# Optimization experiments

Hardware: AMD Instinct MI355X
Metric: run time of the kernel (lower is better)

The kernel has to match this reference:

```python
import jax, jax.numpy as jnp
import numpy as np

N = 100000       # num nodes
E = 3200000      # num edges (avg degree 32)
F_IN = 128       # num_node_features
HID = 16         # hidden dim hard-coded in Net
C = 10           # num_classes


def setup_inputs() -> dict:
    key = jax.random.key(0)
    k1, k2, k3, k4 = jax.random.split(key, 4)
    x = jax.random.normal(k1, (N, F_IN), dtype=jnp.float32)
    edge_index = jax.random.randint(k2, (2, E), 0, N, dtype=jnp.int32)
    W1 = jax.random.normal(k3, (F_IN, HID), dtype=jnp.float32) * 0.05
    b1 = jnp.zeros((HID,), dtype=jnp.float32)
    W2 = jax.random.normal(k4, (HID, C), dtype=jnp.float32) * 0.05
    b2 = jnp.zeros((C,), dtype=jnp.float32)
    return {"x": x, "edge_index": edge_index, "W1": W1, "b1": b1, "W2": W2, "b2": b2}


def reference(x, edge_index, W1, b1, W2, b2):
    # GCNConv: out = D^{-1/2} (A + I) D^{-1/2} X W + b   (add self-loops)
    loops = jnp.arange(N, dtype=edge_index.dtype)
    row = jnp.concatenate([edge_index[0], loops])  # source nodes
    col = jnp.concatenate([edge_index[1], loops])  # target nodes

    # symmetric normalization (degrees include self-loops, so deg >= 1)
    deg = jax.ops.segment_sum(jnp.ones_like(col, dtype=jnp.float32), col, num_segments=N)
    dis = jax.lax.rsqrt(deg)
    norm = dis[row] * dis[col]  # [E+N]

    def gcn_conv(h, W, b):
        h = h @ W                               # [N, d_out] small GEMM first
        msg = h[row] * norm[:, None]            # gather + scale, [E+N, d_out]
        out = jax.ops.segment_sum(msg, col, num_segments=N)  # scatter-add
        return out + b

    h = jax.nn.relu(gcn_conv(x, W1, b1))
    # F.dropout(training=False) is identity in eval mode
    logits = gcn_conv(h, W2, b2)
    return jax.nn.log_softmax(logits, axis=1)
```

## Files before the change

kernel.cpp:

```cpp
#include <hip/hip_runtime.h>
#include <math.h>

#define N_NODES 100000
#define N_EDGES 3200000
#define F_IN 128
#define HID 16
#define C_OUT 10
#define WIN 256
#define NDIG 391
#define PNB2 500
#define EPB 6400
#define SCN (NDIG * PNB2)
#define SB1 764
#define MAXE2 20
#define CSRLDS 10240

typedef unsigned short u16;
typedef unsigned int u32;

__device__ __forceinline__ float bf2f(u16 u) {
    return __uint_as_float(((u32)u) << 16);
}
__device__ __forceinline__ u16 f2bf(float f) {
    u32 x = __float_as_uint(f);
    u32 r = (x + 0x7fffu + ((x >> 16) & 1u)) >> 16;
    return (u16)r;
}
__device__ __forceinline__ void acc8(float* a, uint4 w) {
    a[0] += bf2f((u16)(w.x & 0xffff)); a[1] += bf2f((u16)(w.x >> 16));
    a[2] += bf2f((u16)(w.y & 0xffff)); a[3] += bf2f((u16)(w.y >> 16));
    a[4] += bf2f((u16)(w.z & 0xffff)); a[5] += bf2f((u16)(w.z >> 16));
    a[6] += bf2f((u16)(w.w & 0xffff)); a[7] += bf2f((u16)(w.w >> 16));
}

__global__ void k_pcnt(const int* __restrict__ col, int* __restrict__ blkhistA) {
    __shared__ int h[NDIG];
    for (int i = threadIdx.x; i < NDIG; i += 256) h[i] = 0;
    __syncthreads();
    const uint4* c4 = (const uint4*)(col + blockIdx.x * EPB);
    for (int i = threadIdx.x; i < EPB / 4; i += 256) {
        uint4 c = c4[i];
        atomicAdd(&h[c.x >> 8], 1);
        atomicAdd(&h[c.y >> 8], 1);
        atomicAdd(&h[c.z >> 8], 1);
        atomicAdd(&h[c.w >> 8], 1);
    }
    __syncthreads();
    for (int d = threadIdx.x; d < NDIG; d += 256)
        blkhistA[d * PNB2 + blockIdx.x] = h[d];
}

__global__ void k_s1(const int* __restrict__ blkhistA, int* __restrict__ psum) {
    __shared__ int sm[256];
    int i = blockIdx.x * 256 + threadIdx.x;
    sm[threadIdx.x] = (i < SCN) ? blkhistA[i] : 0;
    __syncthreads();
    for (int off = 128; off > 0; off >>= 1) {
        if (threadIdx.x < off) sm[threadIdx.x] += sm[threadIdx.x + off];
        __syncthreads();
    }
    if (threadIdx.x == 0) psum[blockIdx.x] = sm[0];
}

__global__ void k_s3(const int* __restrict__ blkhistA, const int* __restrict__ psum,
                     int* __restrict__ blkhistB) {
    __shared__ int ps[1024];
    __shared__ int sm[256];
    int t = threadIdx.x;
    for (int i = t; i < 1024; i += 256) ps[i] = (i < SB1) ? psum[i] : 0;
    __syncthreads();
    for (int off = 1; off < 1024; off <<= 1) {
        int v[4];
#pragma unroll
        for (int j = 0; j < 4; j++) {
            int idx = t + j * 256;
            v[j] = ps[idx] + ((idx >= off) ? ps[idx - off] : 0);
        }
        __syncthreads();
#pragma unroll
        for (int j = 0; j < 4; j++) ps[t + j * 256] = v[j];
        __syncthreads();
    }
    int bpre = (blockIdx.x > 0) ? ps[blockIdx.x - 1] : 0;

    int i = blockIdx.x * 256 + t;
    int v = (i < SCN) ? blkhistA[i] : 0;
    sm[t] = v;
    __syncthreads();
    for (int off = 1; off < 256; off <<= 1) {
        int a = sm[t];
        int b = (t >= off) ? sm[t - off] : 0;
        __syncthreads();
        sm[t] = a + b;
        __syncthreads();
    }
    if (i < SCN) blkhistB[i] = bpre + sm[t] - v;
}

__global__ void __launch_bounds__(512) k_pwrite(
        const int* __restrict__ row, const int* __restrict__ col,
        const int* __restrict__ blkhistA, const int* __restrict__ blkhistB,
        u32* __restrict__ staging) {
    __shared__ u32 sorted[EPB];
    __shared__ u16 dwin[EPB];
    __shared__ int gbase[NDIG];
    __shared__ int lbase[NDIG];
    __shared__ int lcur[NDIG];
    __shared__ int scan[512];

    int t = threadIdx.x;
    int b = blockIdx.x;
    int hv = 0;
    if (t < NDIG) {
        hv = blkhistA[t * PNB2 + b];
        gbase[t] = blkhistB[t * PNB2 + b];
        lcur[t] = 0;
    }
    scan[t] = hv;
    __syncthreads();
    for (int off = 1; off < 512; off <<= 1) {
        int v = scan[t];
        int u = (t >= off) ? scan[t - off] : 0;
        __syncthreads();
        scan[t] = v + u;
        __syncthreads();
    }
    if (t < NDIG) lbase[t] = scan[t] - hv;
    __syncthreads();

    const uint4* c4 = (const uint4*)(col + b * EPB);
    const uint4* r4 = (const uint4*)(row + b * EPB);
    for (int i = t; i < EPB / 4; i += 512) {
        uint4 c = c4[i];
        uint4 r = r4[i];
        int d, rank, pos;
        d = (int)(c.x >> 8); rank = atomicAdd(&lcur[d], 1); pos = lbase[d] + rank;
        sorted[pos] = ((c.x & 255u) << 17) | r.x; dwin[pos] = (u16)d;
        d = (int)(c.y >> 8); rank = atomicAdd(&lcur[d], 1); pos = lbase[d] + rank;
        sorted[pos] = ((c.y & 255u) << 17) | r.y; dwin[pos] = (u16)d;
        d = (int)(c.z >> 8); rank = atomicAdd(&lcur[d], 1); pos = lbase[d] + rank;
        sorted[pos] = ((c.z & 255u) << 17) | r.z; dwin[pos] = (u16)d;
        d = (int)(c.w >> 8); rank = atomicAdd(&lcur[d], 1); pos = lbase[d] + rank;
        sorted[pos] = ((c.w & 255u) << 17) | r.w; dwin[pos] = (u16)d;
    }
    __syncthreads();

    for (int i = t; i < EPB; i += 512) {
        int d = dwin[i];
        staging[gbase[d] + (i - lbase[d])] = sorted[i];
    }
}

__global__ void __launch_bounds__(256) k_gemm1d(
        const float* __restrict__ x, const float* __restrict__ W1,
        const u32* __restrict__ staging, const int* __restrict__ blkhistB,
        float* __restrict__ dis, u16* __restrict__ h1s) {
    __shared__ float Ws[F_IN * HID];
    __shared__ int cnt[WIN];
    int w = blockIdx.x;
    int t = threadIdx.x;
    for (int i = t; i < F_IN * HID; i += 256) Ws[i] = W1[i];
    cnt[t] = 0;
    __syncthreads();
    int start = blkhistB[w * PNB2];
    int end = (w == NDIG - 1) ? N_EDGES : blkhistB[(w + 1) * PNB2];
    int head = (4 - (start & 3)) & 3;
    if (head > end - start) head = end - start;
    if (t < head) atomicAdd(&cnt[staging[start + t] >> 17], 1);
    int abody = start + head;
    int nb = (end - abody) >> 2;
    const uint4* s4 = (const uint4*)(staging + abody);
    for (int i = t; i < nb; i += 256) {
        uint4 e = s4[i];
        atomicAdd(&cnt[e.x >> 17], 1);
        atomicAdd(&cnt[e.y >> 17], 1);
        atomicAdd(&cnt[e.z >> 17], 1);
        atomicAdd(&cnt[e.w >> 17], 1);
    }
    int tstart = abody + (nb << 2);
    if (t < end - tstart) atomicAdd(&cnt[staging[tstart + t] >> 17], 1);
    __syncthreads();

    int node = w * WIN + t;
    if (node >= N_NODES) return;
    float d = rsqrtf(1.0f + (float)cnt[t]);
    dis[node] = d;

    float acc[HID];
#pragma unroll
    for (int j = 0; j < HID; j++) acc[j] = 0.f;

    const float4* xr = (const float4*)(x + (size_t)node * F_IN);
#pragma unroll 2
    for (int k4 = 0; k4 < F_IN / 4; k4++) {
        float4 v = xr[k4];
        float xv[4] = {v.x, v.y, v.z, v.w};
#pragma unroll
        for (int kk = 0; kk < 4; kk++) {
            const float4* wr = (const float4*)(Ws + (k4 * 4 + kk) * HID);
            float4 w0 = wr[0], w1 = wr[1], w2 = wr[2], w3 = wr[3];
            float xs = xv[kk];
            acc[0]  += xs * w0.x; acc[1]  += xs * w0.y; acc[2]  += xs * w0.z; acc[3]  += xs * w0.w;
            acc[4]  += xs * w1.x; acc[5]  += xs * w1.y; acc[6]  += xs * w1.z; acc[7]  += xs * w1.w;
            acc[8]  += xs * w2.x; acc[9]  += xs * w2.y; acc[10] += xs * w2.z; acc[11] += xs * w2.w;
            acc[12] += xs * w3.x; acc[13] += xs * w3.y; acc[14] += xs * w3.z; acc[15] += xs * w3.w;
        }
    }

    u32 p[8];
#pragma unroll
    for (int i = 0; i < 8; i++)
        p[i] = (u32)f2bf(acc[2 * i] * d) | ((u32)f2bf(acc[2 * i + 1] * d) << 16);
    u32* dst = (u32*)(h1s + (size_t)node * HID);
#pragma unroll
    for (int i = 0; i < 8; i++) dst[i] = p[i];
}

__global__ void __launch_bounds__(512) k_gl1f(
        u32* staging, const int* __restrict__ blkhistB,
        const u16* __restrict__ h1s, const float* __restrict__ b1,
        const float* __restrict__ W2,
        int* __restrict__ offs, uint4* __restrict__ h2a, u32* __restrict__ h2b) {
    __shared__ u32 sorted[CSRLDS];
    __shared__ int cnt[WIN];
    __shared__ int sbase[WIN];
    __shared__ int cur[WIN];
    __shared__ float Ws[HID * C_OUT];
    __shared__ float b1s[HID];
    int w = blockIdx.x;
    int t = threadIdx.x;
    if (t < HID * C_OUT) Ws[t] = W2[t];
    if (t < HID) b1s[t] = b1[t];
    if (t < WIN) cnt[t] = 0;
    __syncthreads();
    int start = blkhistB[w * PNB2];
    int end = (w == NDIG - 1) ? N_EDGES : blkhistB[(w + 1) * PNB2];
    int m = end - start;
    u32 buf[MAXE2];
    int n = 0;
#pragma unroll
    for (int k = 0; k < MAXE2; k++) {
        int i = k * 512 + t;
        if (i < m) {
            u32 e = staging[start + i];
            buf[k] = e;
            n = k + 1;
            atomicAdd(&cnt[e >> 17], 1);
        }
    }
    __syncthreads();
    if (t < WIN) sbase[t] = cnt[t];
    __syncthreads();
    for (int off = 1; off < WIN; off <<= 1) {
        int v = 0;
        if (t < WIN) {
            v = sbase[t];
            if (t >= off) v += sbase[t - off];
        }
        __syncthreads();
        if (t < WIN) sbase[t] = v;
        __syncthreads();
    }
    if (t < WIN) {
        int excl = sbase[t] - cnt[t];
        sbase[t] = excl;
        cur[t] = excl;
        int node = w * WIN + t;
        if (node < N_NODES) offs[node] = start + excl;
    }
    if (w == 0 && t == 0) offs[N_NODES] = N_EDGES;
    __syncthreads();
#pragma unroll
    for (int k = 0; k < MAXE2; k++) {
        if (k < n) {
            u32 e = buf[k];
            int pos = atomicAdd(&cur[(int)(e >> 17)], 1);
            sorted[pos] = e;
        }
    }
    __syncthreads();
    for (int i = t; i < m; i += 512)
        staging[start + i] = sorted[i];

    const uint4* hb = (const uint4*)h1s;
    int half = (t >> 2) & 1;
    int eq = t & 3;
#pragma unroll 1
    for (int rep = 0; rep < 4; rep++) {
        int nl = rep * 64 + (t >> 3);
        int node = w * WIN + nl;
        bool valid = node < N_NODES;
        float a[8] = {0.f, 0.f, 0.f, 0.f, 0.f, 0.f, 0.f, 0.f};
        int deg = valid ? cnt[nl] : 0;
        int s0 = sbase[nl];
        if (valid && eq == 0) acc8(a, hb[(size_t)node * 2 + half]);
        int lo = s0 + ((deg * eq) >> 2);
        int hi = s0 + ((deg * (eq + 1)) >> 2);
        int j = lo;
        for (; j + 4 <= hi; j += 4) {
            u32 e0 = sorted[j], e1 = sorted[j + 1], e2 = sorted[j + 2], e3 = sorted[j + 3];
            uint4 w0 = hb[(size_t)(e0 & 0x1FFFFu) * 2 + half];
            uint4 w1 = hb[(size_t)(e1 & 0x1FFFFu) * 2 + half];
            uint4 w2 = hb[(size_t)(e2 & 0x1FFFFu) * 2 + half];
            uint4 w3 = hb[(size_t)(e3 & 0x1FFFFu) * 2 + half];
            acc8(a, w0); acc8(a, w1); acc8(a, w2); acc8(a, w3);
        }
        for (; j < hi; j++)
            acc8(a, hb[(size_t)(sorted[j] & 0x1FFFFu) * 2 + half]);

#pragma unroll
        for (int k = 0; k < 8; k++) {
            a[k] += __shfl_xor(a[k], 1);
            a[k] += __shfl_xor(a[k], 2);
        }

        float dc = rsqrtf(1.0f + (float)deg);
        float own[8], oth[8];
#pragma unroll
        for (int k = 0; k < 8; k++) own[k] = a[k] * dc;
#pragma unroll
        for (int k = 0; k < 8; k++) oth[k] = __shfl_xor(own[k], 4);
        float h[16];
#pragma unroll
        for (int k = 0; k < 8; k++) {
            h[k]     = half ? oth[k] : own[k];
            h[8 + k] = half ? own[k] : oth[k];
        }
#pragma unroll
        for (int jj = 0; jj < 16; jj++) h[jj] = fmaxf(h[jj] + b1s[jj], 0.f);

        int nf = half ? 2 : 8;
        float outv[8];
#pragma unroll
        for (int k = 0; k < 8; k++) {
            float s = 0.f;
            if (k < nf) {
                int kk = half * 8 + k;
#pragma unroll
                for (int jj = 0; jj < 16; jj++) s += h[jj] * Ws[jj * C_OUT + kk];
            }
            outv[k] = s * dc;
        }
        if (valid && eq == 0) {
            if (half == 0) {
                uint4 ov;
                ov.x = (u32)f2bf(outv[0]) | ((u32)f2bf(outv[1]) << 16);
                ov.y = (u32)f2bf(outv[2]) | ((u32)f2bf(outv[3]) << 16);
                ov.z = (u32)f2bf(outv[4]) | ((u32)f2bf(outv[5]) << 16);
                ov.w = (u32)f2bf(outv[6]) | ((u32)f2bf(outv[7]) << 16);
                h2a[node] = ov;
            } else {
                h2b[node] = (u32)f2bf(outv[0]) | ((u32)f2bf(outv[1]) << 16);
            }
        }
    }
}

__global__ void k_gather2(const int* __restrict__ offs, const u32* __restrict__ csr,
                          const float* __restrict__ dis, const uint4* __restrict__ h2a,
                          const u32* __restrict__ h2b,
                          const float* __restrict__ b2, float* __restrict__ out) {
    __shared__ float b2s[C_OUT];
    if (threadIdx.x < C_OUT) b2s[threadIdx.x] = b2[threadIdx.x];
    __syncthreads();

    int t = blockIdx.x * 256 + threadIdx.x;
    if (t >= N_NODES * 8) return;
    int node = t >> 3;
    int q = t & 7;
    int half = q >> 2;
    int eq = q & 3;
    float a[8] = {0.f, 0.f, 0.f, 0.f, 0.f, 0.f, 0.f, 0.f};
    if (eq == 0) {
        if (half == 0) {
            acc8(a, h2a[node]);
        } else {
            u32 sc = h2b[node];
            a[0] += bf2f((u16)(sc & 0xffff));
            a[1] += bf2f((u16)(sc >> 16));
        }
    }
    int o = offs[node + half];
    int oo = __shfl_xor(o, 4);
    int s0 = half ? oo : o;
    int s1 = half ? o : oo;
    int len = s1 - s0;
    int lo = s0 + ((len * eq) >> 2);
    int hi = s0 + ((len * (eq + 1)) >> 2);
    int j = lo;
    for (; j < hi && (j & 3); j++) {
        u32 src = csr[j] & 0x1FFFFu;
        if (half == 0) {
            acc8(a, h2a[src]);
        } else {
            u32 v = h2b[src];
            a[0] += bf2f((u16)(v & 0xffff));
            a[1] += bf2f((u16)(v >> 16));
        }
    }
    for (; j + 4 <= hi; j += 4) {
        uint4 ss = *(const uint4*)(csr + j);
        u32 i0 = ss.x & 0x1FFFFu, i1 = ss.y & 0x1FFFFu;
        u32 i2 = ss.z & 0x1FFFFu, i3 = ss.w & 0x1FFFFu;
        if (half == 0) {
            uint4 w0 = h2a[i0];
            uint4 w1 = h2a[i1];
            uint4 w2 = h2a[i2];
            uint4 w3 = h2a[i3];
            acc8(a, w0); acc8(a, w1); acc8(a, w2); acc8(a, w3);
        } else {
            u32 v0 = h2b[i0], v1 = h2b[i1], v2 = h2b[i2], v3 = h2b[i3];
            a[0] += bf2f((u16)(v0 & 0xffff)); a[1] += bf2f((u16)(v0 >> 16));
            a[0] += bf2f((u16)(v1 & 0xffff)); a[1] += bf2f((u16)(v1 >> 16));
            a[0] += bf2f((u16)(v2 & 0xffff)); a[1] += bf2f((u16)(v2 >> 16));
            a[0] += bf2f((u16)(v3 & 0xffff)); a[1] += bf2f((u16)(v3 >> 16));
        }
    }
    for (; j < hi; j++) {
        u32 src = csr[j] & 0x1FFFFu;
        if (half == 0) {
            acc8(a, h2a[src]);
        } else {
            u32 v = h2b[src];
            a[0] += bf2f((u16)(v & 0xffff));
            a[1] += bf2f((u16)(v >> 16));
        }
    }

#pragma unroll
    for (int k = 0; k < 8; k++) {
        a[k] += __shfl_xor(a[k], 1);
        a[k] += __shfl_xor(a[k], 2);
    }

    float dc = dis[node];
    int nf = half ? 2 : 8;
    int fb = half * 8;
    float lg[8];
    float m = -1e30f;
#pragma unroll
    for (int k = 0; k < 8; k++) {
        if (k < nf) {
            lg[k] = a[k] * dc + b2s[fb + k];
            m = fmaxf(m, lg[k]);
        }
    }
    m = fmaxf(m, __shfl_xor(m, 4));
    float s = 0.f;
#pragma unroll
    for (int k = 0; k < 8; k++)
        if (k < nf) s += expf(lg[k] - m);
    s += __shfl_xor(s, 4);
    float ls = logf(s) + m;
    if (eq == 0) {
        float* dst = out + (size_t)node * C_OUT + half * 8;
        if (half == 0) {
#pragma unroll
            for (int i = 0; i < 4; i++)
                *(float2*)(dst + 2 * i) = make_float2(lg[2 * i] - ls, lg[2 * i + 1] - ls);
        } else {
            *(float2*)dst = make_float2(lg[0] - ls, lg[1] - ls);
        }
    }
}

extern "C" void kernel_launch(void* const* d_in, const int* in_sizes, int n_in,
                              void* d_out, int out_size, void* d_ws, size_t ws_size,
                              hipStream_t stream) {
    const float* x  = (const float*)d_in[0];
    const int*   ei = (const int*)d_in[1];
    const float* W1 = (const float*)d_in[2];
    const float* b1 = (const float*)d_in[3];
    const float* W2 = (const float*)d_in[4];
    const float* b2 = (const float*)d_in[5];
    float* out = (float*)d_out;

    const int* row = ei;
    const int* col = ei + N_EDGES;

    char* ws = (char*)d_ws;
    float* dis      = (float*)(ws);
    int*   offs     = (int*)(ws + 400000);
    int*   blkhistA = (int*)(ws + 800016);
    int*   blkhistB = (int*)(ws + 1582352);
    int*   psum     = (int*)(ws + 2364688);
    u32*   staging  = (u32*)(ws + 2367744);
    u16*   h1s      = (u16*)(ws + 15167744);
    uint4* h2a      = (uint4*)(ws + 18367744);
    u32*   h2b      = (u32*)(ws + 19967744);

    const int B = 256;
    int gN8 = (N_NODES * 8 + B - 1) / B;

    k_pcnt  <<<PNB2, B, 0, stream>>>(col, blkhistA);
    k_s1    <<<SB1, B, 0, stream>>>(blkhistA, psum);
    k_s3    <<<SB1, B, 0, stream>>>(blkhistA, psum, blkhistB);
    k_pwrite<<<PNB2, 512, 0, stream>>>(row, col, blkhistA, blkhistB, staging);
    k_gemm1d<<<NDIG, B, 0, stream>>>(x, W1, staging, blkhistB, dis, h1s);
    k_gl1f  <<<NDIG, 512, 0, stream>>>(staging, blkhistB, h1s, b1, W2, offs, h2a, h2b);
    k_gather2<<<gN8, B, 0, stream>>>(offs, staging, dis, h2a, h2b, b2, out);
}
```

Before: 213.8 us.

## Overlap layer-1 GEMM with histogram pass and compute degrees via global atomics

Merges the column histogram kernel with the X·W1 GEMM into one launch of heterogeneous blocks, so the dense GEMM runs alongside the edge histogram instead of after the partition write. Degrees are now counted with global atomics during the histogram pass rather than from the sorted staging buffer. The dis scaling and bf16 packing move into a second kernel that also holds the partial-sum reduction. In exchange it adds 3.2M global atomics, a memset, and an fp32 intermediate written and read back through memory.

```diff
diff --git a/kernel.cpp b/kernel.cpp
--- a/kernel.cpp
+++ b/kernel.cpp
@@ -33,33 +33,99 @@
     a[6] += bf2f((u16)(w.w & 0xffff)); a[7] += bf2f((u16)(w.w >> 16));
 }
 
-__global__ void k_pcnt(const int* __restrict__ col, int* __restrict__ blkhistA) {
-    __shared__ int h[NDIG];
-    for (int i = threadIdx.x; i < NDIG; i += 256) h[i] = 0;
-    __syncthreads();
-    const uint4* c4 = (const uint4*)(col + blockIdx.x * EPB);
-    for (int i = threadIdx.x; i < EPB / 4; i += 256) {
-        uint4 c = c4[i];
-        atomicAdd(&h[c.x >> 8], 1);
-        atomicAdd(&h[c.y >> 8], 1);
-        atomicAdd(&h[c.z >> 8], 1);
-        atomicAdd(&h[c.w >> 8], 1);
-    }
-    __syncthreads();
-    for (int d = threadIdx.x; d < NDIG; d += 256)
-        blkhistA[d * PNB2 + blockIdx.x] = h[d];
-}
-
-__global__ void k_s1(const int* __restrict__ blkhistA, int* __restrict__ psum) {
-    __shared__ int sm[256];
-    int i = blockIdx.x * 256 + threadIdx.x;
-    sm[threadIdx.x] = (i < SCN) ? blkhistA[i] : 0;
-    __syncthreads();
-    for (int off = 128; off > 0; off >>= 1) {
-        if (threadIdx.x < off) sm[threadIdx.x] += sm[threadIdx.x + off];
-        __syncthreads();
-    }
-    if (threadIdx.x == 0) psum[blockIdx.x] = sm[0];
+__global__ void __launch_bounds__(256) k_front(
+        const int* __restrict__ col, const float* __restrict__ x,
+        const float* __restrict__ W1,
+        int* __restrict__ blkhistA, u32* __restrict__ deg, float* __restrict__ h1u) {
+    __shared__ float WsF[F_IN * HID];
+    int t = threadIdx.x;
+    if (blockIdx.x < PNB2) {
+        int* h = (int*)WsF;
+        for (int i = t; i < NDIG; i += 256) h[i] = 0;
+        __syncthreads();
+        const uint4* c4 = (const uint4*)(col + blockIdx.x * EPB);
+        for (int i = t; i < EPB / 4; i += 256) {
+            uint4 c = c4[i];
+            atomicAdd(&h[c.x >> 8], 1);
+            atomicAdd(&h[c.y >> 8], 1);
+            atomicAdd(&h[c.z >> 8], 1);
+            atomicAdd(&h[c.w >> 8], 1);
+            atomicAdd(&deg[c.x], 1u);
+            atomicAdd(&deg[c.y], 1u);
+            atomicAdd(&deg[c.z], 1u);
+            atomicAdd(&deg[c.w], 1u);
+        }
+        __syncthreads();
+        for (int d = t; d < NDIG; d += 256)
+            blkhistA[d * PNB2 + blockIdx.x] = h[d];
+    } else {
+        for (int i = t; i < F_IN * HID; i += 256) WsF[i] = W1[i];
+        __syncthreads();
+        int node = (blockIdx.x - PNB2) * 256 + t;
+        if (node >= N_NODES) return;
+
+        float acc[HID];
+#pragma unroll
+        for (int j = 0; j < HID; j++) acc[j] = 0.f;
+        const float4* xr = (const float4*)(x + (size_t)node * F_IN);
+#pragma unroll 2
+        for (int k4 = 0; k4 < F_IN / 4; k4++) {
+            float4 v = xr[k4];
+            float xv[4] = {v.x, v.y, v.z, v.w};
+#pragma unroll
+            for (int kk = 0; kk < 4; kk++) {
+                const float4* wr = (const float4*)(WsF + (k4 * 4 + kk) * HID);
+                float4 w0 = wr[0], w1 = wr[1], w2 = wr[2], w3 = wr[3];
+                float xs = xv[kk];
+                acc[0]  += xs * w0.x; acc[1]  += xs * w0.y; acc[2]  += xs * w0.z; acc[3]  += xs * w0.w;
+                acc[4]  += xs * w1.x; acc[5]  += xs * w1.y; acc[6]  += xs * w1.z; acc[7]  += xs * w1.w;
+                acc[8]  += xs * w2.x; acc[9]  += xs * w2.y; acc[10] += xs * w2.z; acc[11] += xs * w2.w;
+                acc[12] += xs * w3.x; acc[13] += xs * w3.y; acc[14] += xs * w3.z; acc[15] += xs * w3.w;
+            }
+        }
+        float4* dst = (float4*)(h1u + (size_t)node * HID);
+#pragma unroll
+        for (int i = 0; i < 4; i++)
+            dst[i] = make_float4(acc[4 * i], acc[4 * i + 1], acc[4 * i + 2], acc[4 * i + 3]);
+    }
+}
+
+__global__ void __launch_bounds__(256) k_mid(
+        const int* __restrict__ blkhistA, int* __restrict__ psum,
+        const u32* __restrict__ deg, const float* __restrict__ h1u,
+        float* __restrict__ dis, u16* __restrict__ h1s) {
+    int t = threadIdx.x;
+    if (blockIdx.x < SB1) {
+        __shared__ int sm[256];
+        int i = blockIdx.x * 256 + t;
+        sm[t] = (i < SCN) ? blkhistA[i] : 0;
+        __syncthreads();
+        for (int off = 128; off > 0; off >>= 1) {
+            if (t < off) sm[t] += sm[t + off];
+            __syncthreads();
+        }
+        if (t == 0) psum[blockIdx.x] = sm[0];
+    } else {
+        int node = (blockIdx.x - SB1) * 256 + t;
+        if (node >= N_NODES) return;
+        float d = rsqrtf(1.0f + (float)deg[node]);
+        dis[node] = d;
+        const float4* src = (const float4*)(h1u + (size_t)node * HID);
+        float4 v0 = src[0], v1 = src[1], v2 = src[2], v3 = src[3];
+        float v[16] = {v0.x, v0.y, v0.z, v0.w, v1.x, v1.y, v1.z, v1.w,
+                       v2.x, v2.y, v2.z, v2.w, v3.x, v3.y, v3.z, v3.w};
+        uint4 p0, p1;
+        p0.x = (u32)f2bf(v[0] * d)  | ((u32)f2bf(v[1] * d) << 16);
+        p0.y = (u32)f2bf(v[2] * d)  | ((u32)f2bf(v[3] * d) << 16);
+        p0.z = (u32)f2bf(v[4] * d)  | ((u32)f2bf(v[5] * d) << 16);
+        p0.w = (u32)f2bf(v[6] * d)  | ((u32)f2bf(v[7] * d) << 16);
+        p1.x = (u32)f2bf(v[8] * d)  | ((u32)f2bf(v[9] * d) << 16);
+        p1.y = (u32)f2bf(v[10] * d) | ((u32)f2bf(v[11] * d) << 16);
+        p1.z = (u32)f2bf(v[12] * d) | ((u32)f2bf(v[13] * d) << 16);
+        p1.w = (u32)f2bf(v[14] * d) | ((u32)f2bf(v[15] * d) << 16);
+        uint4* dst = (uint4*)(h1s + (size_t)node * HID);
+        dst[0] = p0; dst[1] = p1;
+    }
 }
 
 __global__ void k_s3(const int* __restrict__ blkhistA, const int* __restrict__ psum,
@@ -149,71 +215,6 @@
         int d = dwin[i];
         staging[gbase[d] + (i - lbase[d])] = sorted[i];
     }
-}
-
-__global__ void __launch_bounds__(256) k_gemm1d(
-        const float* __restrict__ x, const float* __restrict__ W1,
-        const u32* __restrict__ staging, const int* __restrict__ blkhistB,
-        float* __restrict__ dis, u16* __restrict__ h1s) {
-    __shared__ float Ws[F_IN * HID];
-    __shared__ int cnt[WIN];
-    int w = blockIdx.x;
-    int t = threadIdx.x;
-    for (int i = t; i < F_IN * HID; i += 256) Ws[i] = W1[i];
-    cnt[t] = 0;
-    __syncthreads();
-    int start = blkhistB[w * PNB2];
-    int end = (w == NDIG - 1) ? N_EDGES : blkhistB[(w + 1) * PNB2];
-    int head = (4 - (start & 3)) & 3;
-    if (head > end - start) head = end - start;
-    if (t < head) atomicAdd(&cnt[staging[start + t] >> 17], 1);
-    int abody = start + head;
-    int nb = (end - abody) >> 2;
-    const uint4* s4 = (const uint4*)(staging + abody);
-    for (int i = t; i < nb; i += 256) {
-        uint4 e = s4[i];
-        atomicAdd(&cnt[e.x >> 17], 1);
-        atomicAdd(&cnt[e.y >> 17], 1);
-        atomicAdd(&cnt[e.z >> 17], 1);
-        atomicAdd(&cnt[e.w >> 17], 1);
-    }
-    int tstart = abody + (nb << 2);
-    if (t < end - tstart) atomicAdd(&cnt[staging[tstart + t] >> 17], 1);
-    __syncthreads();
-
-    int node = w * WIN + t;
-    if (node >= N_NODES) return;
-    float d = rsqrtf(1.0f + (float)cnt[t]);
-    dis[node] = d;
-
-    float acc[HID];
-#pragma unroll
-    for (int j = 0; j < HID; j++) acc[j] = 0.f;
-
-    const float4* xr = (const float4*)(x + (size_t)node * F_IN);
-#pragma unroll 2
-    for (int k4 = 0; k4 < F_IN / 4; k4++) {
-        float4 v = xr[k4];
-        float xv[4] = {v.x, v.y, v.z, v.w};
-#pragma unroll
-        for (int kk = 0; kk < 4; kk++) {
-            const float4* wr = (const float4*)(Ws + (k4 * 4 + kk) * HID);
-            float4 w0 = wr[0], w1 = wr[1], w2 = wr[2], w3 = wr[3];
-            float xs = xv[kk];
-            acc[0]  += xs * w0.x; acc[1]  += xs * w0.y; acc[2]  += xs * w0.z; acc[3]  += xs * w0.w;
-            acc[4]  += xs * w1.x; acc[5]  += xs * w1.y; acc[6]  += xs * w1.z; acc[7]  += xs * w1.w;
-            acc[8]  += xs * w2.x; acc[9]  += xs * w2.y; acc[10] += xs * w2.z; acc[11] += xs * w2.w;
-            acc[12] += xs * w3.x; acc[13] += xs * w3.y; acc[14] += xs * w3.z; acc[15] += xs * w3.w;
-        }
-    }
-
-    u32 p[8];
-#pragma unroll
-    for (int i = 0; i < 8; i++)
-        p[i] = (u32)f2bf(acc[2 * i] * d) | ((u32)f2bf(acc[2 * i + 1] * d) << 16);
-    u32* dst = (u32*)(h1s + (size_t)node * HID);
-#pragma unroll
-    for (int i = 0; i < 8; i++) dst[i] = p[i];
 }
 
 __global__ void __launch_bounds__(512) k_gl1f(
@@ -488,15 +489,17 @@
     u16*   h1s      = (u16*)(ws + 15167744);
     uint4* h2a      = (uint4*)(ws + 18367744);
     u32*   h2b      = (u32*)(ws + 19967744);
+    u32*   deg      = (u32*)(ws + 20367744);
+    float* h1u      = (float*)(ws + 20767744);
 
     const int B = 256;
     int gN8 = (N_NODES * 8 + B - 1) / B;
 
-    k_pcnt  <<<PNB2, B, 0, stream>>>(col, blkhistA);
-    k_s1    <<<SB1, B, 0, stream>>>(blkhistA, psum);
+    hipMemsetAsync(deg, 0, N_NODES * sizeof(u32), stream);
+    k_front <<<PNB2 + NDIG, B, 0, stream>>>(col, x, W1, blkhistA, deg, h1u);
+    k_mid   <<<SB1 + NDIG, B, 0, stream>>>(blkhistA, psum, deg, h1u, dis, h1s);
     k_s3    <<<SB1, B, 0, stream>>>(blkhistA, psum, blkhistB);
     k_pwrite<<<PNB2, 512, 0, stream>>>(row, col, blkhistA, blkhistB, staging);
-    k_gemm1d<<<NDIG, B, 0, stream>>>(x, W1, staging, blkhistB, dis, h1s);
     k_gl1f  <<<NDIG, 512, 0, stream>>>(staging, blkhistB, h1s, b1, W2, offs, h2a, h2b);
     k_gather2<<<gN8, B, 0, stream>>>(offs, staging, dis, h2a, h2b, b2, out);
 }
```

New measurement: 331.4 us. 1.55x slower.
